# Performance work log

Hardware: AMD Instinct MI355X
Metric: run time of the kernel (lower is better)

## Reference

```python
import jax, jax.numpy as jnp
import numpy as np

NQ, NT, D = 2048, 131072, 64   # query nodes, target nodes, feature dim
E = 2_000_000                  # candidate (u, v) edges
M = 1024                       # consensus (nn_map) pairs; vc = top M rows of Xt


def setup_inputs() -> dict:
    key = jax.random.key(0)
    ks = jax.random.split(key, 8)
    Xq = jax.random.normal(ks[0], (NQ, D), dtype=jnp.float32)
    Xt = jax.random.normal(ks[1], (NT, D), dtype=jnp.float32)
    W_alpha = jax.random.normal(ks[2], (D, D), dtype=jnp.float32) * 0.05
    b_alpha = jax.random.normal(ks[3], (1,), dtype=jnp.float32) * 0.05
    W_beta = jax.random.normal(ks[4], (D, D), dtype=jnp.float32) * 0.05
    b_beta = jax.random.normal(ks[5], (1,), dtype=jnp.float32) * 0.05
    u_idx = jax.random.randint(ks[6], (E,), 0, NQ, dtype=jnp.int32)
    # candidate targets live in [0, NT - M); consensus targets in [NT - M, NT)
    v_idx = jax.random.randint(ks[7], (E,), 0, NT - M, dtype=jnp.int32)
    uc = jax.random.randint(jax.random.fold_in(key, 7), (M,), 0, NQ, dtype=jnp.int32)
    vc = (NT - M) + jnp.arange(M, dtype=jnp.int32)
    return {"Xq": Xq, "Xt": Xt, "W_alpha": W_alpha, "b_alpha": b_alpha,
            "W_beta": W_beta, "b_beta": b_beta,
            "u_idx": u_idx, "v_idx": v_idx, "uc": uc, "vc": vc}


def reference(Xq, Xt, W_alpha, b_alpha, W_beta, b_beta, u_idx, v_idx, uc, vc):
    # 1) consensus overwrite: Xt[vc] = Xq[uc]  (nn_map)
    Xt_c = Xt.at[vc].set(Xq[uc])

    # 2) per-edge gather + bilinear interaction scoring
    xq_e = Xq[u_idx]      # [E, D]
    xt_e = Xt_c[v_idx]    # [E, D]

    def bilinear(W, b):
        return jnp.einsum('ed,df,ef->e', xq_e, W, xt_e) + b[0]

    beta = jax.nn.sigmoid(bilinear(W_beta, b_beta))   # [E] gate
    alpha = jax.nn.elu(bilinear(W_alpha, b_alpha))    # [E] score
    h_e = (1.0 - beta)[:, None] * xq_e + beta[:, None] * xt_e  # [E, D]

    # 3) segment softmax over incoming u per target v (== masked softmax over Nq)
    m = jax.ops.segment_max(alpha, v_idx, num_segments=NT)     # -inf on empty segments
    a = jnp.exp(alpha - m[v_idx])
    s = jax.ops.segment_sum(a, v_idx, num_segments=NT)
    a = a / s[v_idx] + 1e-10   # matches original +1e-10 after normalization

    # 4) scatter-aggregate weighted messages back into Xt rows with >=1 candidate
    agg = jax.ops.segment_sum(a[:, None] * h_e, v_idx, num_segments=NT)  # [NT, D]
    deg = jax.ops.segment_sum(jnp.ones_like(alpha), v_idx, num_segments=NT)
    Xt_out = jnp.where((deg > 0)[:, None], agg, Xt_c)
    return (Xq, Xt_out)
```

## Files before the change

### kernel.cpp

```cpp
#include <hip/hip_runtime.h>

#define NQ 2048
#define NT 131072
#define DD 64
#define MM 1024
#define NBUCK 512
#define BCAP 4608
#define CHUNK 4096

__global__ void yq_kernel(const float* __restrict__ Xq,
                          const float* __restrict__ Wa,
                          const float* __restrict__ Wb,
                          float* __restrict__ Yab) {
    int r = blockIdx.x * 4 + (threadIdx.x >> 6);
    int j = threadIdx.x & 63;
    float sa = 0.f, sb = 0.f;
#pragma unroll
    for (int k = 0; k < DD; ++k) {
        float x = Xq[r * DD + k];
        sa = fmaf(x, Wa[k * DD + j], sa);
        sb = fmaf(x, Wb[k * DD + j], sb);
    }
    Yab[r * 2 * DD + j] = sa;
    Yab[r * 2 * DD + DD + j] = sb;
}

__global__ __launch_bounds__(1024) void bin_kernel(
        const int* __restrict__ u_idx, const int* __restrict__ v_idx,
        int* __restrict__ gcur, unsigned* __restrict__ gbuf, int E) {
    __shared__ unsigned stage[CHUNK];
    __shared__ int hist[NBUCK], off[NBUCK], base[NBUCK], cur[NBUCK];
    int tid = threadIdx.x;
    int e0 = blockIdx.x * CHUNK;
    int n = min(CHUNK, E - e0);
    if (n <= 0) return;

    for (int i = tid; i < NBUCK; i += 1024) hist[i] = 0;
    __syncthreads();

    unsigned p[4];
    int nv = 0;
    int i0 = tid * 4;
    if (i0 + 3 < n) {
        int4 u4 = *(const int4*)(u_idx + e0 + i0);
        int4 v4 = *(const int4*)(v_idx + e0 + i0);
        p[0] = ((unsigned)v4.x << 11) | (unsigned)u4.x;
        p[1] = ((unsigned)v4.y << 11) | (unsigned)u4.y;
        p[2] = ((unsigned)v4.z << 11) | (unsigned)u4.z;
        p[3] = ((unsigned)v4.w << 11) | (unsigned)u4.w;
        nv = 4;
    } else {
        for (int j = 0; j < 4; ++j) {
            if (i0 + j < n) {
                p[j] = ((unsigned)v_idx[e0 + i0 + j] << 11) | (unsigned)u_idx[e0 + i0 + j];
                ++nv;
            }
        }
    }
    for (int j = 0; j < nv; ++j) atomicAdd(&hist[p[j] >> 19], 1);
    __syncthreads();
    if (tid < 64) {
        int h[8], sum = 0;
#pragma unroll
        for (int j = 0; j < 8; ++j) { h[j] = hist[8 * tid + j]; sum += h[j]; }
        int incl = sum;
#pragma unroll
        for (int d = 1; d < 64; d <<= 1) {
            int y = __shfl_up(incl, d, 64);
            if (tid >= d) incl += y;
        }
        int excl = incl - sum;
#pragma unroll
        for (int j = 0; j < 8; ++j) { off[8 * tid + j] = excl; excl += h[j]; }
    }
    __syncthreads();
    for (int i = tid; i < NBUCK; i += 1024) {
        base[i] = hist[i] ? atomicAdd(&gcur[i], hist[i]) : 0;
        cur[i] = off[i];
    }
    __syncthreads();
    for (int j = 0; j < nv; ++j) {
        int pos = atomicAdd(&cur[p[j] >> 19], 1);
        stage[pos] = p[j];
    }
    __syncthreads();
    for (int i = tid; i < n; i += 1024) {
        unsigned q = stage[i];
        int b = q >> 19;
        int idx = base[b] + (i - off[b]);
        if (idx < BCAP) gbuf[(size_t)b * BCAP + idx] = q;
    }
}

#define DOT4(a, b) fmaf((a).x, (b).x, fmaf((a).y, (b).y, fmaf((a).z, (b).z, (a).w * (b).w)))

template <int CTRL>
__device__ __forceinline__ float dpp_add(float x) {
    int xi = __builtin_bit_cast(int, x);
    int yi = __builtin_amdgcn_update_dpp(xi, xi, CTRL, 0xF, 0xF, false);
    return x + __builtin_bit_cast(float, yi);
}
__device__ __forceinline__ float red16(float x) {
    x = dpp_add<0xB1>(x);
    x = dpp_add<0x4E>(x);
    x = dpp_add<0x124>(x);
    x = dpp_add<0x128>(x);
    return x;
}

__global__ __launch_bounds__(1024, 2) void bucket_kernel(
        const float* __restrict__ Xq,
        const float* __restrict__ Xt,
        const float* __restrict__ Yab,
        const float* __restrict__ ba,
        const float* __restrict__ bb,
        const int* __restrict__ gcur,
        const unsigned* __restrict__ gbuf,
        const int* __restrict__ uc,
        float* __restrict__ outXt) {
    __shared__ unsigned short su[BCAP];
    __shared__ int hist[256], cur[256], rstart[257];
    int tid = threadIdx.x;
    int b = blockIdx.x;
    int n = min(gcur[b], BCAP);

    if (tid < 256) hist[tid] = 0;
    __syncthreads();
    for (int i = tid; i < n; i += 1024)
        atomicAdd(&hist[(gbuf[(size_t)b * BCAP + i] >> 11) & 255], 1);
    __syncthreads();
    if (tid < 64) {
        int h0 = hist[4 * tid], h1 = hist[4 * tid + 1];
        int h2 = hist[4 * tid + 2], h3 = hist[4 * tid + 3];
        int tot = h0 + h1 + h2 + h3;
        int incl = tot;
#pragma unroll
        for (int d = 1; d < 64; d <<= 1) {
            int y = __shfl_up(incl, d, 64);
            if (tid >= d) incl += y;
        }
        int excl = incl - tot;
        rstart[4 * tid] = excl;             cur[4 * tid] = excl;
        rstart[4 * tid + 1] = excl + h0;    cur[4 * tid + 1] = excl + h0;
        rstart[4 * tid + 2] = excl + h0 + h1;      cur[4 * tid + 2] = excl + h0 + h1;
        rstart[4 * tid + 3] = excl + h0 + h1 + h2; cur[4 * tid + 3] = excl + h0 + h1 + h2;
        if (tid == 63) rstart[256] = excl + tot;
    }
    __syncthreads();
    for (int i = tid; i < n; i += 1024) {
        unsigned p = gbuf[(size_t)b * BCAP + i];
        int pos = atomicAdd(&cur[(p >> 11) & 255], 1);
        su[pos] = (unsigned short)(p & 0x7FFu);
    }
    __syncthreads();

    int lane = tid & 63;
    int w = tid >> 6;
    int l16 = lane & 15;
    int g = lane >> 4;
    float ba0 = ba[0], bb0 = bb[0];

    for (int r = w; r < 256; r += 16) {
        int v = (b << 8) + r;
        int startr = rstart[r];
        int deg = rstart[r + 1] - startr;
        if (deg == 0) {
            if (g == 0) {
                float4 o;
                if (v >= NT - MM) {
                    int u = uc[v - (NT - MM)];
                    o = ((const float4*)(Xq + (size_t)u * DD))[l16];
                } else {
                    o = ((const float4*)(Xt + (size_t)v * DD))[l16];
                }
                ((float4*)(outXt + (size_t)v * DD))[l16] = o;
            }
            continue;
        }
        float4 xt4 = ((const float4*)(Xt + (size_t)v * DD))[l16];
        float4 acc = make_float4(0.f, 0.f, 0.f, 0.f);
        float s = 0.f;
        for (int base = 0; base < deg; base += 8) {
            int e0 = base + g;
            int e1 = base + 4 + g;
            bool ok0 = e0 < deg, ok1 = e1 < deg;
            int u0 = (int)su[startr + (ok0 ? e0 : 0)];
            int u1 = (int)su[startr + (ok1 ? e1 : 0)];
            const float4* Y0 = (const float4*)(Yab + u0 * (2 * DD));
            const float4* Y1 = (const float4*)(Yab + u1 * (2 * DD));
            float4 ya0 = Y0[l16], yb0 = Y0[16 + l16];
            float4 ya1 = Y1[l16], yb1 = Y1[16 + l16];
            float pa0 = DOT4(ya0, xt4), pb0 = DOT4(yb0, xt4);
            float pa1 = DOT4(ya1, xt4), pb1 = DOT4(yb1, xt4);
            pa0 = red16(pa0); pb0 = red16(pb0);
            pa1 = red16(pa1); pb1 = red16(pb1);
            float la0 = pa0 + ba0, la1 = pa1 + ba0;
            float t0 = __expf(la0), t1 = __expf(la1);
            float al0 = la0 > 0.f ? la0 : (t0 - 1.f);
            float al1 = la1 > 0.f ? la1 : (t1 - 1.f);
            float a0 = ok0 ? __expf(al0) : 0.f;
            float a1 = ok1 ? __expf(al1) : 0.f;
            float be0 = __builtin_amdgcn_rcpf(1.f + __expf(-(pb0 + bb0)));
            float be1 = __builtin_amdgcn_rcpf(1.f + __expf(-(pb1 + bb0)));
            float4 xq0 = ((const float4*)(Xq + (size_t)u0 * DD))[l16];
            float4 xq1 = ((const float4*)(Xq + (size_t)u1 * DD))[l16];
            float4 h0, h1;
            h0.x = fmaf(be0, xt4.x - xq0.x, xq0.x);
            h0.y = fmaf(be0, xt4.y - xq0.y, xq0.y);
            h0.z = fmaf(be0, xt4.z - xq0.z, xq0.z);
            h0.w = fmaf(be0, xt4.w - xq0.w, xq0.w);
            h1.x = fmaf(be1, xt4.x - xq1.x, xq1.x);
            h1.y = fmaf(be1, xt4.y - xq1.y, xq1.y);
            h1.z = fmaf(be1, xt4.z - xq1.z, xq1.z);
            h1.w = fmaf(be1, xt4.w - xq1.w, xq1.w);
            acc.x = fmaf(a0, h0.x, fmaf(a1, h1.x, acc.x));
            acc.y = fmaf(a0, h0.y, fmaf(a1, h1.y, acc.y));
            acc.z = fmaf(a0, h0.z, fmaf(a1, h1.z, acc.z));
            acc.w = fmaf(a0, h0.w, fmaf(a1, h1.w, acc.w));
            s += a0 + a1;
        }
        acc.x += __shfl_xor(acc.x, 16, 64);
        acc.y += __shfl_xor(acc.y, 16, 64);
        acc.z += __shfl_xor(acc.z, 16, 64);
        acc.w += __shfl_xor(acc.w, 16, 64);
        s     += __shfl_xor(s, 16, 64);
        acc.x += __shfl_xor(acc.x, 32, 64);
        acc.y += __shfl_xor(acc.y, 32, 64);
        acc.z += __shfl_xor(acc.z, 32, 64);
        acc.w += __shfl_xor(acc.w, 32, 64);
        s     += __shfl_xor(s, 32, 64);
        if (g == 0) {
            float inv = __builtin_amdgcn_rcpf(s);
            float4 o = make_float4(acc.x * inv, acc.y * inv, acc.z * inv, acc.w * inv);
            ((float4*)(outXt + (size_t)v * DD))[l16] = o;
        }
    }
}

extern "C" void kernel_launch(void* const* d_in, const int* in_sizes, int n_in,
                              void* d_out, int out_size, void* d_ws, size_t ws_size,
                              hipStream_t stream) {
    const float* Xq = (const float*)d_in[0];
    const float* Xt = (const float*)d_in[1];
    const float* Wa = (const float*)d_in[2];
    const float* ba = (const float*)d_in[3];
    const float* Wb = (const float*)d_in[4];
    const float* bb = (const float*)d_in[5];
    const int* u_idx = (const int*)d_in[6];
    const int* v_idx = (const int*)d_in[7];
    const int* uc = (const int*)d_in[8];
    const int* vc = (const int*)d_in[9];
    const int E = in_sizes[6];
    (void)vc;

    float* out = (float*)d_out;
    float* outXq = out;
    float* outXt = out + NQ * DD;

    char* ws = (char*)d_ws;
    float* Yab = (float*)ws;          ws += (size_t)NQ * 2 * DD * sizeof(float);
    int* gcur = (int*)ws;             ws += NBUCK * sizeof(int);
    ws = (char*)(((size_t)ws + 255) & ~(size_t)255);
    unsigned* gbuf = (unsigned*)ws;   ws += (size_t)NBUCK * BCAP * sizeof(unsigned);

    hipMemcpyAsync(outXq, Xq, NQ * DD * sizeof(float), hipMemcpyDeviceToDevice, stream);
    hipMemsetAsync(gcur, 0, NBUCK * sizeof(int), stream);

    yq_kernel<<<NQ / 4, 256, 0, stream>>>(Xq, Wa, Wb, Yab);

    int nchunks = (E + CHUNK - 1) / CHUNK;
    bin_kernel<<<nchunks, 1024, 0, stream>>>(u_idx, v_idx, gcur, gbuf, E);

    bucket_kernel<<<NBUCK, 1024, 0, stream>>>(Xq, Xt, Yab, ba, bb, gcur, gbuf,
                                              uc, outXt);
}
```

Before: 226.1 us.

## Replace two-level bucket binning with global CSR via histogram, scan and scatter

The two-level binning (coarse 512-bucket chunked bin pass, then per-bucket LDS histogram and sort) is replaced by a full CSR build: a global per-target histogram with atomics, a single-block prefix scan over all targets, and an atomic scatter of 16-bit u indices. The bucket kernel then loads precomputed row offsets and a contiguous edge slice, dropping its in-LDS histogram and sort. The trade is more kernel launches, a serial single-block scan over 131072 entries, and many scattered global atomics and 2-byte writes. The DPP bound_ctrl flag is also changed.

```diff
diff --git a/kernel.cpp b/kernel.cpp
--- a/kernel.cpp
+++ b/kernel.cpp
@@ -4,9 +4,7 @@
 #define NT 131072
 #define DD 64
 #define MM 1024
-#define NBUCK 512
-#define BCAP 4608
-#define CHUNK 4096
+#define SUCAP 5120
 
 __global__ void yq_kernel(const float* __restrict__ Xq,
                           const float* __restrict__ Wa,
@@ -25,70 +23,88 @@
     Yab[r * 2 * DD + DD + j] = sb;
 }
 
-__global__ __launch_bounds__(1024) void bin_kernel(
-        const int* __restrict__ u_idx, const int* __restrict__ v_idx,
-        int* __restrict__ gcur, unsigned* __restrict__ gbuf, int E) {
-    __shared__ unsigned stage[CHUNK];
-    __shared__ int hist[NBUCK], off[NBUCK], base[NBUCK], cur[NBUCK];
-    int tid = threadIdx.x;
-    int e0 = blockIdx.x * CHUNK;
-    int n = min(CHUNK, E - e0);
-    if (n <= 0) return;
-
-    for (int i = tid; i < NBUCK; i += 1024) hist[i] = 0;
-    __syncthreads();
-
-    unsigned p[4];
-    int nv = 0;
-    int i0 = tid * 4;
-    if (i0 + 3 < n) {
-        int4 u4 = *(const int4*)(u_idx + e0 + i0);
-        int4 v4 = *(const int4*)(v_idx + e0 + i0);
-        p[0] = ((unsigned)v4.x << 11) | (unsigned)u4.x;
-        p[1] = ((unsigned)v4.y << 11) | (unsigned)u4.y;
-        p[2] = ((unsigned)v4.z << 11) | (unsigned)u4.z;
-        p[3] = ((unsigned)v4.w << 11) | (unsigned)u4.w;
-        nv = 4;
+__global__ __launch_bounds__(1024) void hist_kernel(const int* __restrict__ v_idx,
+                                                    int* __restrict__ hist, int E) {
+    int i0 = (blockIdx.x * 1024 + threadIdx.x) * 4;
+    if (i0 + 3 < E) {
+        int4 v4 = *(const int4*)(v_idx + i0);
+        atomicAdd(&hist[v4.x], 1);
+        atomicAdd(&hist[v4.y], 1);
+        atomicAdd(&hist[v4.z], 1);
+        atomicAdd(&hist[v4.w], 1);
     } else {
-        for (int j = 0; j < 4; ++j) {
-            if (i0 + j < n) {
-                p[j] = ((unsigned)v_idx[e0 + i0 + j] << 11) | (unsigned)u_idx[e0 + i0 + j];
-                ++nv;
-            }
-        }
-    }
-    for (int j = 0; j < nv; ++j) atomicAdd(&hist[p[j] >> 19], 1);
-    __syncthreads();
-    if (tid < 64) {
-        int h[8], sum = 0;
-#pragma unroll
-        for (int j = 0; j < 8; ++j) { h[j] = hist[8 * tid + j]; sum += h[j]; }
+        for (int j = 0; j < 4; ++j)
+            if (i0 + j < E) atomicAdd(&hist[v_idx[i0 + j]], 1);
+    }
+}
+
+__global__ __launch_bounds__(1024) void scan_kernel(const int* __restrict__ hist,
+                                                    int* __restrict__ rofs,
+                                                    int* __restrict__ cur) {
+    __shared__ int wex[16];
+    __shared__ int blktot;
+    int tid = threadIdx.x, lane = tid & 63, w = tid >> 6;
+    int carry = 0;
+    for (int base = 0; base < NT; base += 4096) {
+        int4 h = ((const int4*)(hist + base))[tid];
+        int s01 = h.x + h.y;
+        int sum = s01 + h.z + h.w;
         int incl = sum;
 #pragma unroll
         for (int d = 1; d < 64; d <<= 1) {
             int y = __shfl_up(incl, d, 64);
-            if (tid >= d) incl += y;
-        }
-        int excl = incl - sum;
+            if (lane >= d) incl += y;
+        }
+        if (lane == 63) wex[w] = incl;
+        __syncthreads();
+        if (tid < 16) {
+            int t = wex[tid];
+            int inc2 = t;
 #pragma unroll
-        for (int j = 0; j < 8; ++j) { off[8 * tid + j] = excl; excl += h[j]; }
-    }
-    __syncthreads();
-    for (int i = tid; i < NBUCK; i += 1024) {
-        base[i] = hist[i] ? atomicAdd(&gcur[i], hist[i]) : 0;
-        cur[i] = off[i];
-    }
-    __syncthreads();
-    for (int j = 0; j < nv; ++j) {
-        int pos = atomicAdd(&cur[p[j] >> 19], 1);
-        stage[pos] = p[j];
-    }
-    __syncthreads();
-    for (int i = tid; i < n; i += 1024) {
-        unsigned q = stage[i];
-        int b = q >> 19;
-        int idx = base[b] + (i - off[b]);
-        if (idx < BCAP) gbuf[(size_t)b * BCAP + idx] = q;
+            for (int d = 1; d < 16; d <<= 1) {
+                int y = __shfl_up(inc2, d, 64);
+                if (tid >= d) inc2 += y;
+            }
+            wex[tid] = inc2 - t;
+            if (tid == 15) blktot = inc2;
+        }
+        __syncthreads();
+        int excl = carry + wex[w] + (incl - sum);
+        int4 o;
+        o.x = excl;
+        o.y = excl + h.x;
+        o.z = excl + s01;
+        o.w = excl + s01 + h.z;
+        ((int4*)(rofs + base))[tid] = o;
+        ((int4*)(cur + base))[tid] = o;
+        carry += blktot;
+        __syncthreads();
+    }
+    if (tid == 0) rofs[NT] = carry;
+}
+
+__global__ __launch_bounds__(1024) void scatter_kernel(
+        const int* __restrict__ u_idx, const int* __restrict__ v_idx,
+        int* __restrict__ cur, unsigned short* __restrict__ eu, int E) {
+    int i0 = (blockIdx.x * 1024 + threadIdx.x) * 4;
+    if (i0 + 3 < E) {
+        int4 u4 = *(const int4*)(u_idx + i0);
+        int4 v4 = *(const int4*)(v_idx + i0);
+        int p0 = atomicAdd(&cur[v4.x], 1);
+        int p1 = atomicAdd(&cur[v4.y], 1);
+        int p2 = atomicAdd(&cur[v4.z], 1);
+        int p3 = atomicAdd(&cur[v4.w], 1);
+        eu[p0] = (unsigned short)u4.x;
+        eu[p1] = (unsigned short)u4.y;
+        eu[p2] = (unsigned short)u4.z;
+        eu[p3] = (unsigned short)u4.w;
+    } else {
+        for (int j = 0; j < 4; ++j) {
+            if (i0 + j < E) {
+                int pos = atomicAdd(&cur[v_idx[i0 + j]], 1);
+                eu[pos] = (unsigned short)u_idx[i0 + j];
+            }
+        }
     }
 }
 
@@ -97,7 +113,7 @@
 template <int CTRL>
 __device__ __forceinline__ float dpp_add(float x) {
     int xi = __builtin_bit_cast(int, x);
-    int yi = __builtin_amdgcn_update_dpp(xi, xi, CTRL, 0xF, 0xF, false);
+    int yi = __builtin_amdgcn_update_dpp(xi, xi, CTRL, 0xF, 0xF, true);
     return x + __builtin_bit_cast(float, yi);
 }
 __device__ __forceinline__ float red16(float x) {
@@ -114,44 +130,20 @@
         const float* __restrict__ Yab,
         const float* __restrict__ ba,
         const float* __restrict__ bb,
-        const int* __restrict__ gcur,
-        const unsigned* __restrict__ gbuf,
+        const int* __restrict__ rofs,
+        const unsigned short* __restrict__ eu,
         const int* __restrict__ uc,
         float* __restrict__ outXt) {
-    __shared__ unsigned short su[BCAP];
-    __shared__ int hist[256], cur[256], rstart[257];
+    __shared__ unsigned short su[SUCAP];
+    __shared__ int rstart[257];
     int tid = threadIdx.x;
     int b = blockIdx.x;
-    int n = min(gcur[b], BCAP);
-
-    if (tid < 256) hist[tid] = 0;
+
+    if (tid <= 256) rstart[tid] = rofs[(b << 8) + tid];
     __syncthreads();
-    for (int i = tid; i < n; i += 1024)
-        atomicAdd(&hist[(gbuf[(size_t)b * BCAP + i] >> 11) & 255], 1);
-    __syncthreads();
-    if (tid < 64) {
-        int h0 = hist[4 * tid], h1 = hist[4 * tid + 1];
-        int h2 = hist[4 * tid + 2], h3 = hist[4 * tid + 3];
-        int tot = h0 + h1 + h2 + h3;
-        int incl = tot;
-#pragma unroll
-        for (int d = 1; d < 64; d <<= 1) {
-            int y = __shfl_up(incl, d, 64);
-            if (tid >= d) incl += y;
-        }
-        int excl = incl - tot;
-        rstart[4 * tid] = excl;             cur[4 * tid] = excl;
-        rstart[4 * tid + 1] = excl + h0;    cur[4 * tid + 1] = excl + h0;
-        rstart[4 * tid + 2] = excl + h0 + h1;      cur[4 * tid + 2] = excl + h0 + h1;
-        rstart[4 * tid + 3] = excl + h0 + h1 + h2; cur[4 * tid + 3] = excl + h0 + h1 + h2;
-        if (tid == 63) rstart[256] = excl + tot;
-    }
-    __syncthreads();
-    for (int i = tid; i < n; i += 1024) {
-        unsigned p = gbuf[(size_t)b * BCAP + i];
-        int pos = atomicAdd(&cur[(p >> 11) & 255], 1);
-        su[pos] = (unsigned short)(p & 0x7FFu);
-    }
+    int estart = rstart[0];
+    int ecnt = min(rstart[256] - estart, SUCAP);
+    for (int i = tid; i < ecnt; i += 1024) su[i] = eu[estart + i];
     __syncthreads();
 
     int lane = tid & 63;
@@ -162,8 +154,9 @@
 
     for (int r = w; r < 256; r += 16) {
         int v = (b << 8) + r;
-        int startr = rstart[r];
-        int deg = rstart[r + 1] - startr;
+        int s0 = rstart[r] - estart;
+        int deg = rstart[r + 1] - rstart[r];
+        deg = min(deg, max(0, ecnt - s0));
         if (deg == 0) {
             if (g == 0) {
                 float4 o;
@@ -184,8 +177,8 @@
             int e0 = base + g;
             int e1 = base + 4 + g;
             bool ok0 = e0 < deg, ok1 = e1 < deg;
-            int u0 = (int)su[startr + (ok0 ? e0 : 0)];
-            int u1 = (int)su[startr + (ok1 ? e1 : 0)];
+            int u0 = (int)su[s0 + (ok0 ? e0 : 0)];
+            int u1 = (int)su[s0 + (ok1 ? e1 : 0)];
             const float4* Y0 = (const float4*)(Yab + u0 * (2 * DD));
             const float4* Y1 = (const float4*)(Yab + u1 * (2 * DD));
             float4 ya0 = Y0[l16], yb0 = Y0[16 + l16];
@@ -258,19 +251,23 @@
     float* outXt = out + NQ * DD;
 
     char* ws = (char*)d_ws;
-    float* Yab = (float*)ws;          ws += (size_t)NQ * 2 * DD * sizeof(float);
-    int* gcur = (int*)ws;             ws += NBUCK * sizeof(int);
+    float* Yab = (float*)ws;            ws += (size_t)NQ * 2 * DD * sizeof(float);
+    int* hist = (int*)ws;               ws += (size_t)NT * sizeof(int);
+    int* rofs = (int*)ws;               ws += (size_t)(NT + 1) * sizeof(int);
     ws = (char*)(((size_t)ws + 255) & ~(size_t)255);
-    unsigned* gbuf = (unsigned*)ws;   ws += (size_t)NBUCK * BCAP * sizeof(unsigned);
+    int* cur = (int*)ws;                ws += (size_t)NT * sizeof(int);
+    unsigned short* eu = (unsigned short*)ws;  ws += (size_t)(E + 4) * sizeof(unsigned short);
 
     hipMemcpyAsync(outXq, Xq, NQ * DD * sizeof(float), hipMemcpyDeviceToDevice, stream);
-    hipMemsetAsync(gcur, 0, NBUCK * sizeof(int), stream);
+    hipMemsetAsync(hist, 0, (size_t)NT * sizeof(int), stream);
 
     yq_kernel<<<NQ / 4, 256, 0, stream>>>(Xq, Wa, Wb, Yab);
 
-    int nchunks = (E + CHUNK - 1) / CHUNK;
-    bin_kernel<<<nchunks, 1024, 0, stream>>>(u_idx, v_idx, gcur, gbuf, E);
-
-    bucket_kernel<<<NBUCK, 1024, 0, stream>>>(Xq, Xt, Yab, ba, bb, gcur, gbuf,
-                                              uc, outXt);
-}
+    int nblk = (E + 4095) / 4096;
+    hist_kernel<<<nblk, 1024, 0, stream>>>(v_idx, hist, E);
+    scan_kernel<<<1, 1024, 0, stream>>>(hist, rofs, cur);
+    scatter_kernel<<<nblk, 1024, 0, stream>>>(u_idx, v_idx, cur, eu, E);
+
+    bucket_kernel<<<NT / 256, 1024, 0, stream>>>(Xq, Xt, Yab, ba, bb, rofs, eu,
+                                                 uc, outXt);
+}
```

Result: slower. 476.0 us (+110.5%).

## Replace per-bucket counting sort with LDS atomic accumulation per target row

Applied to the files above, without the earlier changes.

Drops the in-block histogram, prefix scan and counting sort of bucket edges. Each edge is now processed directly in arrival order and its weighted message is accumulated into an LDS row accumulator with float atomics, followed by a normalization pass. This removes the sort phases and their barriers, but it adds five LDS atomics per edge lane, reloads the Xt row for every edge instead of once per target, and accumulates in nondeterministic order. The DPP bound_ctrl flag is also switched to true.

```diff
diff --git a/kernel.cpp b/kernel.cpp
--- a/kernel.cpp
+++ b/kernel.cpp
@@ -97,7 +97,7 @@
 template <int CTRL>
 __device__ __forceinline__ float dpp_add(float x) {
     int xi = __builtin_bit_cast(int, x);
-    int yi = __builtin_amdgcn_update_dpp(xi, xi, CTRL, 0xF, 0xF, false);
+    int yi = __builtin_amdgcn_update_dpp(xi, xi, CTRL, 0xF, 0xF, true);
     return x + __builtin_bit_cast(float, yi);
 }
 __device__ __forceinline__ float red16(float x) {
@@ -118,40 +118,14 @@
         const unsigned* __restrict__ gbuf,
         const int* __restrict__ uc,
         float* __restrict__ outXt) {
-    __shared__ unsigned short su[BCAP];
-    __shared__ int hist[256], cur[256], rstart[257];
+    __shared__ float accl[256 * 65];
+    __shared__ float sacc[256];
     int tid = threadIdx.x;
     int b = blockIdx.x;
     int n = min(gcur[b], BCAP);
 
-    if (tid < 256) hist[tid] = 0;
-    __syncthreads();
-    for (int i = tid; i < n; i += 1024)
-        atomicAdd(&hist[(gbuf[(size_t)b * BCAP + i] >> 11) & 255], 1);
-    __syncthreads();
-    if (tid < 64) {
-        int h0 = hist[4 * tid], h1 = hist[4 * tid + 1];
-        int h2 = hist[4 * tid + 2], h3 = hist[4 * tid + 3];
-        int tot = h0 + h1 + h2 + h3;
-        int incl = tot;
-#pragma unroll
-        for (int d = 1; d < 64; d <<= 1) {
-            int y = __shfl_up(incl, d, 64);
-            if (tid >= d) incl += y;
-        }
-        int excl = incl - tot;
-        rstart[4 * tid] = excl;             cur[4 * tid] = excl;
-        rstart[4 * tid + 1] = excl + h0;    cur[4 * tid + 1] = excl + h0;
-        rstart[4 * tid + 2] = excl + h0 + h1;      cur[4 * tid + 2] = excl + h0 + h1;
-        rstart[4 * tid + 3] = excl + h0 + h1 + h2; cur[4 * tid + 3] = excl + h0 + h1 + h2;
-        if (tid == 63) rstart[256] = excl + tot;
-    }
-    __syncthreads();
-    for (int i = tid; i < n; i += 1024) {
-        unsigned p = gbuf[(size_t)b * BCAP + i];
-        int pos = atomicAdd(&cur[(p >> 11) & 255], 1);
-        su[pos] = (unsigned short)(p & 0x7FFu);
-    }
+    for (int i = tid; i < 256 * 65; i += 1024) accl[i] = 0.f;
+    if (tid < 256) sacc[tid] = 0.f;
     __syncthreads();
 
     int lane = tid & 63;
@@ -159,81 +133,58 @@
     int l16 = lane & 15;
     int g = lane >> 4;
     float ba0 = ba[0], bb0 = bb[0];
+    const unsigned* gb = gbuf + (size_t)b * BCAP;
+
+    int rounds = (n + 63) >> 6;
+    for (int t = 0; t < rounds; ++t) {
+        int i = (t << 6) + (w << 2) + g;
+        bool ok = i < n;
+        unsigned p = gb[ok ? i : 0];
+        int v = (int)(p >> 11);
+        int u = (int)(p & 0x7FFu);
+        const float4* Y = (const float4*)(Yab + (u << 7));
+        float4 ya = Y[l16];
+        float4 yb = Y[16 + l16];
+        float4 xt4 = ((const float4*)(Xt + ((size_t)v << 6)))[l16];
+        float4 xq4 = ((const float4*)(Xq + (u << 6)))[l16];
+        float pa = DOT4(ya, xt4);
+        float pb = DOT4(yb, xt4);
+        pa = red16(pa);
+        pb = red16(pb);
+        float la = pa + ba0;
+        float tt = __expf(la);
+        float al = la > 0.f ? la : (tt - 1.f);
+        float a = __expf(al);
+        float be = __builtin_amdgcn_rcpf(1.f + __expf(-(pb + bb0)));
+        float4 ah;
+        ah.x = a * fmaf(be, xt4.x - xq4.x, xq4.x);
+        ah.y = a * fmaf(be, xt4.y - xq4.y, xq4.y);
+        ah.z = a * fmaf(be, xt4.z - xq4.z, xq4.z);
+        ah.w = a * fmaf(be, xt4.w - xq4.w, xq4.w);
+        if (ok) {
+            int r = v & 255;
+            float* ap = accl + r * 65 + (l16 << 2);
+            atomicAdd(ap + 0, ah.x);
+            atomicAdd(ap + 1, ah.y);
+            atomicAdd(ap + 2, ah.z);
+            atomicAdd(ap + 3, ah.w);
+            if (l16 == 0) atomicAdd(&sacc[r], a);
+        }
+    }
+    __syncthreads();
 
     for (int r = w; r < 256; r += 16) {
         int v = (b << 8) + r;
-        int startr = rstart[r];
-        int deg = rstart[r + 1] - startr;
-        if (deg == 0) {
-            if (g == 0) {
-                float4 o;
-                if (v >= NT - MM) {
-                    int u = uc[v - (NT - MM)];
-                    o = ((const float4*)(Xq + (size_t)u * DD))[l16];
-                } else {
-                    o = ((const float4*)(Xt + (size_t)v * DD))[l16];
-                }
-                ((float4*)(outXt + (size_t)v * DD))[l16] = o;
-            }
-            continue;
-        }
-        float4 xt4 = ((const float4*)(Xt + (size_t)v * DD))[l16];
-        float4 acc = make_float4(0.f, 0.f, 0.f, 0.f);
-        float s = 0.f;
-        for (int base = 0; base < deg; base += 8) {
-            int e0 = base + g;
-            int e1 = base + 4 + g;
-            bool ok0 = e0 < deg, ok1 = e1 < deg;
-            int u0 = (int)su[startr + (ok0 ? e0 : 0)];
-            int u1 = (int)su[startr + (ok1 ? e1 : 0)];
-            const float4* Y0 = (const float4*)(Yab + u0 * (2 * DD));
-            const float4* Y1 = (const float4*)(Yab + u1 * (2 * DD));
-            float4 ya0 = Y0[l16], yb0 = Y0[16 + l16];
-            float4 ya1 = Y1[l16], yb1 = Y1[16 + l16];
-            float pa0 = DOT4(ya0, xt4), pb0 = DOT4(yb0, xt4);
-            float pa1 = DOT4(ya1, xt4), pb1 = DOT4(yb1, xt4);
-            pa0 = red16(pa0); pb0 = red16(pb0);
-            pa1 = red16(pa1); pb1 = red16(pb1);
-            float la0 = pa0 + ba0, la1 = pa1 + ba0;
-            float t0 = __expf(la0), t1 = __expf(la1);
-            float al0 = la0 > 0.f ? la0 : (t0 - 1.f);
-            float al1 = la1 > 0.f ? la1 : (t1 - 1.f);
-            float a0 = ok0 ? __expf(al0) : 0.f;
-            float a1 = ok1 ? __expf(al1) : 0.f;
-            float be0 = __builtin_amdgcn_rcpf(1.f + __expf(-(pb0 + bb0)));
-            float be1 = __builtin_amdgcn_rcpf(1.f + __expf(-(pb1 + bb0)));
-            float4 xq0 = ((const float4*)(Xq + (size_t)u0 * DD))[l16];
-            float4 xq1 = ((const float4*)(Xq + (size_t)u1 * DD))[l16];
-            float4 h0, h1;
-            h0.x = fmaf(be0, xt4.x - xq0.x, xq0.x);
-            h0.y = fmaf(be0, xt4.y - xq0.y, xq0.y);
-            h0.z = fmaf(be0, xt4.z - xq0.z, xq0.z);
-            h0.w = fmaf(be0, xt4.w - xq0.w, xq0.w);
-            h1.x = fmaf(be1, xt4.x - xq1.x, xq1.x);
-            h1.y = fmaf(be1, xt4.y - xq1.y, xq1.y);
-            h1.z = fmaf(be1, xt4.z - xq1.z, xq1.z);
-            h1.w = fmaf(be1, xt4.w - xq1.w, xq1.w);
-            acc.x = fmaf(a0, h0.x, fmaf(a1, h1.x, acc.x));
-            acc.y = fmaf(a0, h0.y, fmaf(a1, h1.y, acc.y));
-            acc.z = fmaf(a0, h0.z, fmaf(a1, h1.z, acc.z));
-            acc.w = fmaf(a0, h0.w, fmaf(a1, h1.w, acc.w));
-            s += a0 + a1;
-        }
-        acc.x += __shfl_xor(acc.x, 16, 64);
-        acc.y += __shfl_xor(acc.y, 16, 64);
-        acc.z += __shfl_xor(acc.z, 16, 64);
-        acc.w += __shfl_xor(acc.w, 16, 64);
-        s     += __shfl_xor(s, 16, 64);
-        acc.x += __shfl_xor(acc.x, 32, 64);
-        acc.y += __shfl_xor(acc.y, 32, 64);
-        acc.z += __shfl_xor(acc.z, 32, 64);
-        acc.w += __shfl_xor(acc.w, 32, 64);
-        s     += __shfl_xor(s, 32, 64);
-        if (g == 0) {
-            float inv = __builtin_amdgcn_rcpf(s);
-            float4 o = make_float4(acc.x * inv, acc.y * inv, acc.z * inv, acc.w * inv);
-            ((float4*)(outXt + (size_t)v * DD))[l16] = o;
-        }
+        float sv = sacc[r];
+        float o;
+        if (sv > 0.f) {
+            o = accl[r * 65 + lane] * __builtin_amdgcn_rcpf(sv);
+        } else if (v >= NT - MM) {
+            o = Xq[uc[v - (NT - MM)] * DD + lane];
+        } else {
+            o = Xt[(size_t)v * DD + lane];
+        }
+        outXt[(size_t)v * DD + lane] = o;
     }
 }
 
```

New measurement: 795.7 us. 252% more time.

## Store per-query projections and Xq in fp16, use packed fdot2 for bilinear scores

Applied to the files above, without the earlier changes.

The projected query rows (Yab) and a copy of Xq are now written as half precision, with Ya and Yb interleaved so each lane loads both halves in a single 16-byte read. The edge loop computes the bilinear dot products with packed fp16 dot instructions and converts the Xq values back to float for the message blend. This halves the bytes of the per-edge random gathers and the dot-product instruction count. In exchange, precision drops to fp16 for the logits and messages, which may affect accuracy tolerance. The DPP bound_ctrl flag is also flipped.

```diff
diff --git a/kernel.cpp b/kernel.cpp
--- a/kernel.cpp
+++ b/kernel.cpp
@@ -8,10 +8,28 @@
 #define BCAP 4608
 #define CHUNK 4096
 
+
+typedef __attribute__((ext_vector_type(2))) _Float16 h2;
+
+#if defined(__has_builtin)
+#if __has_builtin(__builtin_amdgcn_fdot2)
+#define HAVE_FDOT2 1
+#endif
+#endif
+
+__device__ __forceinline__ float fdot2(h2 a, h2 b, float c) {
+#ifdef HAVE_FDOT2
+    return __builtin_amdgcn_fdot2(a, b, c, false);
+#else
+    return fmaf((float)a.x, (float)b.x, fmaf((float)a.y, (float)b.y, c));
+#endif
+}
+
 __global__ void yq_kernel(const float* __restrict__ Xq,
                           const float* __restrict__ Wa,
                           const float* __restrict__ Wb,
-                          float* __restrict__ Yab) {
+                          _Float16* __restrict__ Yab16,
+                          _Float16* __restrict__ Xq16) {
     int r = blockIdx.x * 4 + (threadIdx.x >> 6);
     int j = threadIdx.x & 63;
     float sa = 0.f, sb = 0.f;
@@ -21,8 +39,10 @@
         sa = fmaf(x, Wa[k * DD + j], sa);
         sb = fmaf(x, Wb[k * DD + j], sb);
     }
-    Yab[r * 2 * DD + j] = sa;
-    Yab[r * 2 * DD + DD + j] = sb;
+    int gbase = r * 128 + (j >> 2) * 8 + (j & 3);
+    Yab16[gbase] = (_Float16)sa;
+    Yab16[gbase + 4] = (_Float16)sb;
+    Xq16[r * DD + j] = (_Float16)Xq[r * DD + j];
 }
 
 __global__ __launch_bounds__(1024) void bin_kernel(
@@ -92,12 +112,10 @@
     }
 }
 
-#define DOT4(a, b) fmaf((a).x, (b).x, fmaf((a).y, (b).y, fmaf((a).z, (b).z, (a).w * (b).w)))
-
 template <int CTRL>
 __device__ __forceinline__ float dpp_add(float x) {
     int xi = __builtin_bit_cast(int, x);
-    int yi = __builtin_amdgcn_update_dpp(xi, xi, CTRL, 0xF, 0xF, false);
+    int yi = __builtin_amdgcn_update_dpp(xi, xi, CTRL, 0xF, 0xF, true);
     return x + __builtin_bit_cast(float, yi);
 }
 __device__ __forceinline__ float red16(float x) {
@@ -111,7 +129,8 @@
 __global__ __launch_bounds__(1024, 2) void bucket_kernel(
         const float* __restrict__ Xq,
         const float* __restrict__ Xt,
-        const float* __restrict__ Yab,
+        const _Float16* __restrict__ Yab16,
+        const _Float16* __restrict__ Xq16,
         const float* __restrict__ ba,
         const float* __restrict__ bb,
         const int* __restrict__ gcur,
@@ -131,8 +150,8 @@
     __syncthreads();
     if (tid < 64) {
         int h0 = hist[4 * tid], h1 = hist[4 * tid + 1];
-        int h2 = hist[4 * tid + 2], h3 = hist[4 * tid + 3];
-        int tot = h0 + h1 + h2 + h3;
+        int h2_ = hist[4 * tid + 2], h3 = hist[4 * tid + 3];
+        int tot = h0 + h1 + h2_ + h3;
         int incl = tot;
 #pragma unroll
         for (int d = 1; d < 64; d <<= 1) {
@@ -142,8 +161,8 @@
         int excl = incl - tot;
         rstart[4 * tid] = excl;             cur[4 * tid] = excl;
         rstart[4 * tid + 1] = excl + h0;    cur[4 * tid + 1] = excl + h0;
-        rstart[4 * tid + 2] = excl + h0 + h1;      cur[4 * tid + 2] = excl + h0 + h1;
-        rstart[4 * tid + 3] = excl + h0 + h1 + h2; cur[4 * tid + 3] = excl + h0 + h1 + h2;
+        rstart[4 * tid + 2] = excl + h0 + h1;       cur[4 * tid + 2] = excl + h0 + h1;
+        rstart[4 * tid + 3] = excl + h0 + h1 + h2_; cur[4 * tid + 3] = excl + h0 + h1 + h2_;
         if (tid == 63) rstart[256] = excl + tot;
     }
     __syncthreads();
@@ -178,6 +197,9 @@
             continue;
         }
         float4 xt4 = ((const float4*)(Xt + (size_t)v * DD))[l16];
+        h2 xt01, xt23;
+        xt01.x = (_Float16)xt4.x; xt01.y = (_Float16)xt4.y;
+        xt23.x = (_Float16)xt4.z; xt23.y = (_Float16)xt4.w;
         float4 acc = make_float4(0.f, 0.f, 0.f, 0.f);
         float s = 0.f;
         for (int base = 0; base < deg; base += 8) {
@@ -186,12 +208,18 @@
             bool ok0 = e0 < deg, ok1 = e1 < deg;
             int u0 = (int)su[startr + (ok0 ? e0 : 0)];
             int u1 = (int)su[startr + (ok1 ? e1 : 0)];
-            const float4* Y0 = (const float4*)(Yab + u0 * (2 * DD));
-            const float4* Y1 = (const float4*)(Yab + u1 * (2 * DD));
-            float4 ya0 = Y0[l16], yb0 = Y0[16 + l16];
-            float4 ya1 = Y1[l16], yb1 = Y1[16 + l16];
-            float pa0 = DOT4(ya0, xt4), pb0 = DOT4(yb0, xt4);
-            float pa1 = DOT4(ya1, xt4), pb1 = DOT4(yb1, xt4);
+            float4 y0 = ((const float4*)(Yab16 + (u0 << 7)))[l16];
+            float4 y1 = ((const float4*)(Yab16 + (u1 << 7)))[l16];
+            float2 xv0 = ((const float2*)(Xq16 + (u0 << 6)))[l16];
+            float2 xv1 = ((const float2*)(Xq16 + (u1 << 6)))[l16];
+            float pa0 = fdot2(__builtin_bit_cast(h2, y0.y), xt23,
+                       fdot2(__builtin_bit_cast(h2, y0.x), xt01, 0.f));
+            float pb0 = fdot2(__builtin_bit_cast(h2, y0.w), xt23,
+                       fdot2(__builtin_bit_cast(h2, y0.z), xt01, 0.f));
+            float pa1 = fdot2(__builtin_bit_cast(h2, y1.y), xt23,
+                       fdot2(__builtin_bit_cast(h2, y1.x), xt01, 0.f));
+            float pb1 = fdot2(__builtin_bit_cast(h2, y1.w), xt23,
+                       fdot2(__builtin_bit_cast(h2, y1.z), xt01, 0.f));
             pa0 = red16(pa0); pb0 = red16(pb0);
             pa1 = red16(pa1); pb1 = red16(pb1);
             float la0 = pa0 + ba0, la1 = pa1 + ba0;
@@ -202,21 +230,23 @@
             float a1 = ok1 ? __expf(al1) : 0.f;
             float be0 = __builtin_amdgcn_rcpf(1.f + __expf(-(pb0 + bb0)));
             float be1 = __builtin_amdgcn_rcpf(1.f + __expf(-(pb1 + bb0)));
-            float4 xq0 = ((const float4*)(Xq + (size_t)u0 * DD))[l16];
-            float4 xq1 = ((const float4*)(Xq + (size_t)u1 * DD))[l16];
-            float4 h0, h1;
-            h0.x = fmaf(be0, xt4.x - xq0.x, xq0.x);
-            h0.y = fmaf(be0, xt4.y - xq0.y, xq0.y);
-            h0.z = fmaf(be0, xt4.z - xq0.z, xq0.z);
-            h0.w = fmaf(be0, xt4.w - xq0.w, xq0.w);
-            h1.x = fmaf(be1, xt4.x - xq1.x, xq1.x);
-            h1.y = fmaf(be1, xt4.y - xq1.y, xq1.y);
-            h1.z = fmaf(be1, xt4.z - xq1.z, xq1.z);
-            h1.w = fmaf(be1, xt4.w - xq1.w, xq1.w);
-            acc.x = fmaf(a0, h0.x, fmaf(a1, h1.x, acc.x));
-            acc.y = fmaf(a0, h0.y, fmaf(a1, h1.y, acc.y));
-            acc.z = fmaf(a0, h0.z, fmaf(a1, h1.z, acc.z));
-            acc.w = fmaf(a0, h0.w, fmaf(a1, h1.w, acc.w));
+            h2 q0a = __builtin_bit_cast(h2, xv0.x), q0b = __builtin_bit_cast(h2, xv0.y);
+            h2 q1a = __builtin_bit_cast(h2, xv1.x), q1b = __builtin_bit_cast(h2, xv1.y);
+            float x0x = (float)q0a.x, x0y = (float)q0a.y, x0z = (float)q0b.x, x0w = (float)q0b.y;
+            float x1x = (float)q1a.x, x1y = (float)q1a.y, x1z = (float)q1b.x, x1w = (float)q1b.y;
+            float4 h0v, h1v;
+            h0v.x = fmaf(be0, xt4.x - x0x, x0x);
+            h0v.y = fmaf(be0, xt4.y - x0y, x0y);
+            h0v.z = fmaf(be0, xt4.z - x0z, x0z);
+            h0v.w = fmaf(be0, xt4.w - x0w, x0w);
+            h1v.x = fmaf(be1, xt4.x - x1x, x1x);
+            h1v.y = fmaf(be1, xt4.y - x1y, x1y);
+            h1v.z = fmaf(be1, xt4.z - x1z, x1z);
+            h1v.w = fmaf(be1, xt4.w - x1w, x1w);
+            acc.x = fmaf(a0, h0v.x, fmaf(a1, h1v.x, acc.x));
+            acc.y = fmaf(a0, h0v.y, fmaf(a1, h1v.y, acc.y));
+            acc.z = fmaf(a0, h0v.z, fmaf(a1, h1v.z, acc.z));
+            acc.w = fmaf(a0, h0v.w, fmaf(a1, h1v.w, acc.w));
             s += a0 + a1;
         }
         acc.x += __shfl_xor(acc.x, 16, 64);
@@ -258,7 +288,8 @@
     float* outXt = out + NQ * DD;
 
     char* ws = (char*)d_ws;
-    float* Yab = (float*)ws;          ws += (size_t)NQ * 2 * DD * sizeof(float);
+    _Float16* Yab16 = (_Float16*)ws;  ws += (size_t)NQ * 2 * DD * sizeof(_Float16);
+    _Float16* Xq16 = (_Float16*)ws;   ws += (size_t)NQ * DD * sizeof(_Float16);
     int* gcur = (int*)ws;             ws += NBUCK * sizeof(int);
     ws = (char*)(((size_t)ws + 255) & ~(size_t)255);
     unsigned* gbuf = (unsigned*)ws;   ws += (size_t)NBUCK * BCAP * sizeof(unsigned);
@@ -266,11 +297,11 @@
     hipMemcpyAsync(outXq, Xq, NQ * DD * sizeof(float), hipMemcpyDeviceToDevice, stream);
     hipMemsetAsync(gcur, 0, NBUCK * sizeof(int), stream);
 
-    yq_kernel<<<NQ / 4, 256, 0, stream>>>(Xq, Wa, Wb, Yab);
+    yq_kernel<<<NQ / 4, 256, 0, stream>>>(Xq, Wa, Wb, Yab16, Xq16);
 
     int nchunks = (E + CHUNK - 1) / CHUNK;
     bin_kernel<<<nchunks, 1024, 0, stream>>>(u_idx, v_idx, gcur, gbuf, E);
 
-    bucket_kernel<<<NBUCK, 1024, 0, stream>>>(Xq, Xt, Yab, ba, bb, gcur, gbuf,
+    bucket_kernel<<<NBUCK, 1024, 0, stream>>>(Xq, Xt, Yab16, Xq16, ba, bb, gcur, gbuf,
                                               uc, outXt);
 }
```

Result: faster. 207.2 us (-8.3%).
